# Kernel tuning notes

Hardware: AMD Instinct MI355X
Metric: run time of the kernel (lower is better)

## Reference

```python
import jax, jax.numpy as jnp
from jax import lax
import numpy as np

BN_EPS = 1e-3  # ultralytics BatchNorm2d default eps

def setup_inputs() -> dict:
    key = jax.random.key(0)
    ks = jax.random.split(key, 6)
    B, C, H, W = 16, 64, 160, 160
    E, R = 4, 16  # experts, reduced router dim = C // reduction
    return {
        "x": jax.random.normal(ks[0], (B, C, H, W), jnp.float32),
        "fc1_w": jax.random.normal(ks[1], (R, C), jnp.float32) * 0.1,
        "fc2_w": jax.random.normal(ks[2], (E, R), jnp.float32) * 0.1,
        "fc2_b": jax.random.normal(ks[3], (E,), jnp.float32) * 0.1,
        "conv_w": jax.random.normal(ks[4], (E, C, C, 3, 3), jnp.float32) * 0.05,
        "bn_gamma": jnp.ones((E, C), jnp.float32),
        "bn_beta": jnp.zeros((E, C), jnp.float32),
        "bn_mean": jax.random.normal(ks[5], (E, C), jnp.float32) * 0.1,
        "bn_var": jnp.ones((E, C), jnp.float32),
    }

def reference(x, fc1_w, fc2_w, fc2_b, conv_w, bn_gamma, bn_beta, bn_mean, bn_var):
    # Router: global avg pool -> fc1 -> relu -> fc2 -> softmax over experts
    g = jnp.mean(x, axis=(2, 3))                       # [B, C]
    h = jax.nn.relu(g @ fc1_w.T)                       # [B, R]
    w = jax.nn.softmax(h @ fc2_w.T + fc2_b, axis=1)    # [B, E]

    def expert(kernel, gamma, beta, mean, var):
        # Conv2d(bias=False, pad=k//2) + BatchNorm2d (eval) + SiLU
        y = lax.conv_general_dilated(
            x, kernel, window_strides=(1, 1), padding="SAME",
            dimension_numbers=("NCHW", "OIHW", "NCHW"))
        scale = (gamma * lax.rsqrt(var + BN_EPS))[None, :, None, None]
        shift = (beta - mean * gamma * lax.rsqrt(var + BN_EPS))[None, :, None, None]
        return jax.nn.silu(y * scale + shift)          # [B, Co, H, W]

    outs = jax.vmap(expert)(conv_w, bn_gamma, bn_beta, bn_mean, bn_var)  # [E, B, Co, H, W]
    return jnp.einsum("ebchw,be->bchw", outs, w)
```

## Files before the change

### kernel.cpp

```cpp
#include <hip/hip_runtime.h>
#include <hip/hip_bf16.h>

typedef unsigned short u16;
typedef unsigned int   u32;
typedef __attribute__((ext_vector_type(8))) short s16x8;
typedef __attribute__((ext_vector_type(16))) float f32x16;

#define BN_EPS 1e-3f
#define NB 16
#define NC 64
#define NH 160
#define NW 160
#define HP 162
#define WPD 162

#define OFF_XT 0UL
#define SZ_XT  (16UL*162*162*64*2)
#define OFF_WT (OFF_XT + SZ_XT)
#define SZ_WT  (4UL*64*9*64*2)
#define OFF_SC (OFF_WT + SZ_WT)
#define OFF_SH (OFF_SC + 1024UL)
#define OFF_WE (OFF_SH + 1024UL)
#define OFF_GP (OFF_WE + 256UL)

#define XSTRIDE 342
#define XLS_BYTES (8 * XSTRIDE * 16)
#define WLS_BYTES (2304 * 16)
#define SMEM_TOTAL (XLS_BYTES + WLS_BYTES)

__device__ __forceinline__ u16 f2bf(float f) {
    u32 u = __builtin_bit_cast(u32, f);
    u += 0x7fffu + ((u >> 16) & 1u);
    return (u16)(u >> 16);
}

__global__ void prep_all(const float* __restrict__ x, u16* __restrict__ xt,
                         float* __restrict__ gpart,
                         const float* __restrict__ cw, u16* __restrict__ wt,
                         const float* __restrict__ gamma, const float* __restrict__ beta,
                         const float* __restrict__ mean, const float* __restrict__ var,
                         float* __restrict__ scale, float* __restrict__ shift) {
    __shared__ float tile[64][33];
    int blk = blockIdx.x;
    int t = threadIdx.x;
    if (blk >= 15392) {
        int idx = (blk - 15392) * 256 + t;
        {
            int cin = idx & 7;
            int r = idx >> 3;
            int co = r & 63; r >>= 6;
            int cio = r & 3; r >>= 2;
            int tap = r % 9; r /= 9;
            int ch = r & 1;
            int e = r >> 1;
            int ci = ch * 32 + cio * 8 + cin;
            wt[idx] = f2bf(cw[(((long)(e * 64 + co)) * 64 + ci) * 9 + tap]);
        }
        if (idx < 256) {
            float sc = gamma[idx] * rsqrtf(var[idx] + BN_EPS);
            scale[idx] = sc;
            shift[idx] = beta[idx] - mean[idx] * sc;
        }
        return;
    }
    if (blk >= 12800) {
        int bb = blk - 12800;
        int hp = bb % 162, b = bb / 162;
        u32* row = (u32*)xt + (((long)b * 162 + hp) * 162) * 32;
        if (hp == 0 || hp == 161) {
            for (int i = t; i < 162 * 32; i += 256) row[i] = 0u;
        } else if (t < 64) {
            int p = (t >> 5) ? 161 : 0;
            row[p * 32 + (t & 31)] = 0u;
        }
        return;
    }
    int wt5 = blk % 5;
    int tmp = blk / 5;
    int h = tmp % 160, b = tmp / 160;
    int w0 = wt5 * 32;
    int w = t & 31, c0 = t >> 5;
#pragma unroll
    for (int i = 0; i < 8; ++i) {
        int c = c0 + 8 * i;
        tile[c][w] = x[(((long)b * 64 + c) * 160 + h) * 160 + w0 + w];
    }
    __syncthreads();
    if (t < 64) {
        float s = 0.f;
#pragma unroll
        for (int wi = 0; wi < 32; ++wi) s += tile[t][wi];
        gpart[((long)(b * 64 + t)) * 800 + h * 5 + wt5] = s;
    }
    u32* xt32 = (u32*)xt;
    long base = ((((long)b * 162 + h + 1) * 162) + (w0 + 1)) * 32;
#pragma unroll
    for (int j = 0; j < 4; ++j) {
        int idx = t + 256 * j;
        int p = idx >> 5, cp = idx & 31;
        float v0 = tile[2 * cp][p], v1 = tile[2 * cp + 1][p];
        xt32[base + p * 32 + cp] = (u32)f2bf(v0) | ((u32)f2bf(v1) << 16);
    }
}

__global__ void router16(const float* __restrict__ gpart,
                         const float* __restrict__ fc1w, const float* __restrict__ fc2w,
                         const float* __restrict__ fc2b, float* __restrict__ wexp) {
    __shared__ float part[256];
    __shared__ float gl[64];
    __shared__ float h1[16];
    int b = blockIdx.x, t = threadIdx.x;
    int c = t >> 2, q = t & 3;
    const float* gp = gpart + ((long)(b * 64 + c)) * 800;
    float s = 0.f;
    for (int i = q; i < 800; i += 4) s += gp[i];
    part[t] = s;
    __syncthreads();
    if (t < 64)
        gl[t] = (part[4 * t] + part[4 * t + 1] + part[4 * t + 2] + part[4 * t + 3])
                * (1.f / 25600.f);
    __syncthreads();
    if (t < 16) {
        float v = 0.f;
#pragma unroll
        for (int c2 = 0; c2 < 64; ++c2) v += gl[c2] * fc1w[t * 64 + c2];
        h1[t] = fmaxf(v, 0.f);
    }
    __syncthreads();
    if (t == 0) {
        float z[4];
#pragma unroll
        for (int e = 0; e < 4; ++e) {
            float v = fc2b[e];
#pragma unroll
            for (int r = 0; r < 16; ++r) v += h1[r] * fc2w[e * 16 + r];
            z[e] = v;
        }
        float m = fmaxf(fmaxf(z[0], z[1]), fmaxf(z[2], z[3]));
        float e0 = __expf(z[0] - m), e1 = __expf(z[1] - m);
        float e2 = __expf(z[2] - m), e3 = __expf(z[3] - m);
        float inv = 1.f / (e0 + e1 + e2 + e3);
        wexp[b * 4 + 0] = e0 * inv; wexp[b * 4 + 1] = e1 * inv;
        wexp[b * 4 + 2] = e2 * inv; wexp[b * 4 + 3] = e3 * inv;
    }
}

__global__ __launch_bounds__(256, 2) void conv_main(
    const u16* __restrict__ xt, const u16* __restrict__ wt,
    const float* __restrict__ scale, const float* __restrict__ shift,
    const float* __restrict__ wexp, float* __restrict__ out) {
    extern __shared__ char smem[];
    u16* xls = (u16*)smem;
    u16* wls = (u16*)(smem + XLS_BYTES);

    const int o = blockIdx.x;
    const int blk = (o & 7) * 200 + (o >> 3);
    const int wt5 = blk % 5;
    const int tmp = blk / 5;
    const int ht = tmp % 20;
    const int b = tmp / 20;
    const int h0 = ht * 8, w0 = wt5 * 32;
    const int tid = threadIdx.x;
    const int lane = tid & 63;
    const int wv = tid >> 6;
    const int l31 = lane & 31, kh = lane >> 5;
    const int r0 = 2 * wv;

    {
#pragma unroll
        for (int r = 0; r < 9; ++r) {
            int oo = r * 256 + tid;
            __builtin_amdgcn_global_load_lds(
                (const __attribute__((address_space(1))) void*)(wt + oo * 8),
                (__attribute__((address_space(3))) void*)(wls + oo * 8),
                16, 0, 0);
        }
    }
    {
        const u16* xb = xt + (long)b * HP * WPD * 64;
        for (int c = tid; c < 2720; c += 256) {
            int P = c >> 3, cg = c & 7;
            int y = P / 34, px = P - y * 34;
            const u16* src = xb + (((long)(h0 + y) * WPD) + (w0 + px)) * 64 + cg * 8;
            s16x8 v = *(const s16x8*)src;
            *(s16x8*)(&xls[(cg * XSTRIDE + P) << 3]) = v;
        }
    }

    const int oA2 = (kh * 64 + l31) << 3;
    const int oB_0 = ((kh * XSTRIDE) + (r0 + 0) * 34 + l31) << 3;
    const int oB_1 = ((kh * XSTRIDE) + (r0 + 1) * 34 + l31) << 3;

    f32x16 acc00 = (f32x16)(0.f), acc01 = (f32x16)(0.f);
    f32x16 acc10 = (f32x16)(0.f), acc11 = (f32x16)(0.f);
    f32x16 oac00 = (f32x16)(0.f), oac01 = (f32x16)(0.f);
    f32x16 oac10 = (f32x16)(0.f), oac11 = (f32x16)(0.f);

    auto epi = [&](int E) {
        const float we = wexp[(b << 2) + E];
        const float* scE = scale + (E << 6);
        const float* shE = shift + (E << 6);
#pragma unroll
        for (int j = 0; j < 16; ++j) {
            const int cob = (j & 3) + 8 * (j >> 2) + 4 * kh;
            {
                float sc = scE[cob], sh = shE[cob];
                float y0 = acc00[j] * sc + sh;
                float y1 = acc01[j] * sc + sh;
                oac00[j] += we * (y0 * __builtin_amdgcn_rcpf(1.f + __expf(-y0)));
                oac01[j] += we * (y1 * __builtin_amdgcn_rcpf(1.f + __expf(-y1)));
            }
            {
                float sc = scE[cob + 32], sh = shE[cob + 32];
                float y0 = acc10[j] * sc + sh;
                float y1 = acc11[j] * sc + sh;
                oac10[j] += we * (y0 * __builtin_amdgcn_rcpf(1.f + __expf(-y0)));
                oac11[j] += we * (y1 * __builtin_amdgcn_rcpf(1.f + __expf(-y1)));
            }
        }
        acc00 = (f32x16)(0.f); acc01 = (f32x16)(0.f);
        acc10 = (f32x16)(0.f); acc11 = (f32x16)(0.f);
    };

#pragma unroll 1
    for (int s = 0; s < 8; ++s) {
        const int ch = s & 1;
        if (s > 0) {
            __syncthreads();
            const u16* wsrc = wt + ((long)s) * 2304 * 8;
#pragma unroll
            for (int r = 0; r < 9; ++r) {
                int oo = r * 256 + tid;
                __builtin_amdgcn_global_load_lds(
                    (const __attribute__((address_space(1))) void*)(wsrc + oo * 8),
                    (__attribute__((address_space(3))) void*)(wls + oo * 8),
                    16, 0, 0);
            }
        }
        const int oBc0 = oB_0 + ((ch * 4 * XSTRIDE) << 3);
        const int oBc1 = oB_1 + ((ch * 4 * XSTRIDE) << 3);

        auto tap_body = [&](int tap) {
            const int dy = tap / 3, dx = tap - 3 * dy;
            const int pofU = (dy * 34 + dx) << 3;
            const int atU = oA2 + tap * 2048;
            s16x8 a00 = *(const s16x8*)(&wls[atU]);
            s16x8 a10 = *(const s16x8*)(&wls[atU + 256]);
            s16x8 a01 = *(const s16x8*)(&wls[atU + 1024]);
            s16x8 a11 = *(const s16x8*)(&wls[atU + 1280]);
            s16x8 b00 = *(const s16x8*)(&xls[oBc0 + pofU]);
            s16x8 b10 = *(const s16x8*)(&xls[oBc1 + pofU]);
            s16x8 b01 = *(const s16x8*)(&xls[oBc0 + pofU + 2 * XSTRIDE * 8]);
            s16x8 b11 = *(const s16x8*)(&xls[oBc1 + pofU + 2 * XSTRIDE * 8]);
            acc00 = __builtin_amdgcn_mfma_f32_32x32x16_bf16(a00, b00, acc00, 0, 0, 0);
            acc10 = __builtin_amdgcn_mfma_f32_32x32x16_bf16(a10, b00, acc10, 0, 0, 0);
            acc01 = __builtin_amdgcn_mfma_f32_32x32x16_bf16(a00, b10, acc01, 0, 0, 0);
            acc11 = __builtin_amdgcn_mfma_f32_32x32x16_bf16(a10, b10, acc11, 0, 0, 0);
            acc00 = __builtin_amdgcn_mfma_f32_32x32x16_bf16(a01, b01, acc00, 0, 0, 0);
            acc10 = __builtin_amdgcn_mfma_f32_32x32x16_bf16(a11, b01, acc10, 0, 0, 0);
            acc01 = __builtin_amdgcn_mfma_f32_32x32x16_bf16(a01, b11, acc01, 0, 0, 0);
            acc11 = __builtin_amdgcn_mfma_f32_32x32x16_bf16(a11, b11, acc11, 0, 0, 0);
        };

        if (s == 0) __builtin_amdgcn_s_waitcnt(0x070);
        else        __builtin_amdgcn_s_waitcnt(0x074);
        __builtin_amdgcn_s_barrier();
        __builtin_amdgcn_sched_barrier(0);
        if (ch == 0 && s > 0) epi((s >> 1) - 1);
#pragma unroll
        for (int tap = 0; tap < 5; ++tap) tap_body(tap);

        __builtin_amdgcn_s_waitcnt(0xF70);
        __builtin_amdgcn_s_barrier();
        __builtin_amdgcn_sched_barrier(0);
#pragma unroll
        for (int tap = 5; tap < 9; ++tap) tap_body(tap);
    }
    epi(3);

    const int yy = h0 + r0;
#pragma unroll
    for (int j = 0; j < 16; ++j) {
        const int cob = (j & 3) + 8 * (j >> 2) + 4 * kh;
        out[(((long)(b * 64 + cob)) * 160 + yy) * 160 + w0 + l31] = oac00[j];
        out[(((long)(b * 64 + cob)) * 160 + yy + 1) * 160 + w0 + l31] = oac01[j];
        out[(((long)(b * 64 + cob + 32)) * 160 + yy) * 160 + w0 + l31] = oac10[j];
        out[(((long)(b * 64 + cob + 32)) * 160 + yy + 1) * 160 + w0 + l31] = oac11[j];
    }
}

extern "C" void kernel_launch(void* const* d_in, const int* in_sizes, int n_in,
                              void* d_out, int out_size, void* d_ws, size_t ws_size,
                              hipStream_t stream) {
    const float* x = (const float*)d_in[0];
    const float* fc1w = (const float*)d_in[1];
    const float* fc2w = (const float*)d_in[2];
    const float* fc2b = (const float*)d_in[3];
    const float* convw = (const float*)d_in[4];
    const float* gamma = (const float*)d_in[5];
    const float* beta = (const float*)d_in[6];
    const float* mean = (const float*)d_in[7];
    const float* var = (const float*)d_in[8];
    float* out = (float*)d_out;
    char* ws = (char*)d_ws;
    u16* xt = (u16*)(ws + OFF_XT);
    u16* wtb = (u16*)(ws + OFF_WT);
    float* scale = (float*)(ws + OFF_SC);
    float* shift = (float*)(ws + OFF_SH);
    float* wexp = (float*)(ws + OFF_WE);
    float* gpart = (float*)(ws + OFF_GP);

    hipFuncSetAttribute((const void*)conv_main,
                        hipFuncAttributeMaxDynamicSharedMemorySize, SMEM_TOTAL);

    prep_all<<<15968, 256, 0, stream>>>(x, xt, gpart, convw, wtb,
                                        gamma, beta, mean, var, scale, shift);
    router16<<<16, 256, 0, stream>>>(gpart, fc1w, fc2w, fc2b, wexp);
    conv_main<<<1600, 256, SMEM_TOTAL, stream>>>(xt, wtb, scale, shift, wexp, out);
}
```

Before: 194.1 us.

## Reorder conv taps by dx to reuse LDS B-fragments and split router reduction

```diff
diff --git a/kernel.cpp b/kernel.cpp
--- a/kernel.cpp
+++ b/kernel.cpp
@@ -20,7 +20,8 @@
 #define SZ_WT  (4UL*64*9*64*2)
 #define OFF_SC (OFF_WT + SZ_WT)
 #define OFF_SH (OFF_SC + 1024UL)
-#define OFF_WE (OFF_SH + 1024UL)
+#define OFF_G  (OFF_SH + 1024UL)
+#define OFF_WE (OFF_G + 4096UL)
 #define OFF_GP (OFF_WE + 256UL)
 
 #define XSTRIDE 342
@@ -34,35 +35,35 @@
     return (u16)(u >> 16);
 }
 
-__global__ void prep_all(const float* __restrict__ x, u16* __restrict__ xt,
-                         float* __restrict__ gpart,
-                         const float* __restrict__ cw, u16* __restrict__ wt,
-                         const float* __restrict__ gamma, const float* __restrict__ beta,
-                         const float* __restrict__ mean, const float* __restrict__ var,
-                         float* __restrict__ scale, float* __restrict__ shift) {
+__global__ void prep_w(const float* __restrict__ cw, u16* __restrict__ wt,
+                       const float* __restrict__ gamma, const float* __restrict__ beta,
+                       const float* __restrict__ mean, const float* __restrict__ var,
+                       float* __restrict__ scale, float* __restrict__ shift) {
+    int idx = blockIdx.x * 256 + threadIdx.x;
+    if (idx < 4 * 2 * 9 * 4 * 64 * 8) {
+        int cin = idx & 7;
+        int t = idx >> 3;
+        int co = t & 63; t >>= 6;
+        int cio = t & 3; t >>= 2;
+        int pos = t % 9; t /= 9;
+        int ch = t & 1;
+        int e = t >> 1;
+        int tsp = (pos % 3) * 3 + (pos / 3);
+        int ci = ch * 32 + cio * 8 + cin;
+        wt[idx] = f2bf(cw[(((long)(e * 64 + co)) * 64 + ci) * 9 + tsp]);
+    }
+    if (idx < 256) {
+        float sc = gamma[idx] * rsqrtf(var[idx] + BN_EPS);
+        scale[idx] = sc;
+        shift[idx] = beta[idx] - mean[idx] * sc;
+    }
+}
+
+__global__ void prep_x(const float* __restrict__ x, u16* __restrict__ xt,
+                       float* __restrict__ gpart) {
     __shared__ float tile[64][33];
     int blk = blockIdx.x;
     int t = threadIdx.x;
-    if (blk >= 15392) {
-        int idx = (blk - 15392) * 256 + t;
-        {
-            int cin = idx & 7;
-            int r = idx >> 3;
-            int co = r & 63; r >>= 6;
-            int cio = r & 3; r >>= 2;
-            int tap = r % 9; r /= 9;
-            int ch = r & 1;
-            int e = r >> 1;
-            int ci = ch * 32 + cio * 8 + cin;
-            wt[idx] = f2bf(cw[(((long)(e * 64 + co)) * 64 + ci) * 9 + tap]);
-        }
-        if (idx < 256) {
-            float sc = gamma[idx] * rsqrtf(var[idx] + BN_EPS);
-            scale[idx] = sc;
-            shift[idx] = beta[idx] - mean[idx] * sc;
-        }
-        return;
-    }
     if (blk >= 12800) {
         int bb = blk - 12800;
         int hp = bb % 162, b = bb / 162;
@@ -103,42 +104,49 @@
     }
 }
 
-__global__ void router16(const float* __restrict__ gpart,
-                         const float* __restrict__ fc1w, const float* __restrict__ fc2w,
-                         const float* __restrict__ fc2b, float* __restrict__ wexp) {
-    __shared__ float part[256];
-    __shared__ float gl[64];
-    __shared__ float h1[16];
-    int b = blockIdx.x, t = threadIdx.x;
-    int c = t >> 2, q = t & 3;
-    const float* gp = gpart + ((long)(b * 64 + c)) * 800;
+__global__ void g_reduce(const float* __restrict__ gpart, float* __restrict__ g) {
+    int id = blockIdx.x;
+    int t = threadIdx.x;
     float s = 0.f;
-    for (int i = q; i < 800; i += 4) s += gp[i];
-    part[t] = s;
-    __syncthreads();
-    if (t < 64)
-        gl[t] = (part[4 * t] + part[4 * t + 1] + part[4 * t + 2] + part[4 * t + 3])
-                * (1.f / 25600.f);
+    for (int i = t; i < 800; i += 256) s += gpart[(long)id * 800 + i];
+#pragma unroll
+    for (int off = 32; off > 0; off >>= 1) s += __shfl_down(s, off, 64);
+    __shared__ float red[4];
+    if ((t & 63) == 0) red[t >> 6] = s;
+    __syncthreads();
+    if (t == 0) g[id] = (red[0] + red[1] + red[2] + red[3]) * (1.f / 25600.f);
+}
+
+__global__ void router(const float* __restrict__ g, const float* __restrict__ fc1w,
+                       const float* __restrict__ fc2w, const float* __restrict__ fc2b,
+                       float* __restrict__ wexp) {
+    __shared__ float gL[16][64];
+    __shared__ float h1[16][16];
+    __shared__ float z[16][4];
+    int t = threadIdx.x;
+    for (int i = t; i < 1024; i += 256) gL[i >> 6][i & 63] = g[i];
+    __syncthreads();
+    {
+        int b = t >> 4, r = t & 15;
+        float s = 0.f;
+#pragma unroll
+        for (int c = 0; c < 64; ++c) s += gL[b][c] * fc1w[r * 64 + c];
+        h1[b][r] = fmaxf(s, 0.f);
+    }
+    __syncthreads();
+    if (t < 64) {
+        int b = t >> 2, e = t & 3;
+        float s = fc2b[e];
+#pragma unroll
+        for (int r = 0; r < 16; ++r) s += h1[b][r] * fc2w[e * 16 + r];
+        z[b][e] = s;
+    }
     __syncthreads();
     if (t < 16) {
-        float v = 0.f;
-#pragma unroll
-        for (int c2 = 0; c2 < 64; ++c2) v += gl[c2] * fc1w[t * 64 + c2];
-        h1[t] = fmaxf(v, 0.f);
-    }
-    __syncthreads();
-    if (t == 0) {
-        float z[4];
-#pragma unroll
-        for (int e = 0; e < 4; ++e) {
-            float v = fc2b[e];
-#pragma unroll
-            for (int r = 0; r < 16; ++r) v += h1[r] * fc2w[e * 16 + r];
-            z[e] = v;
-        }
-        float m = fmaxf(fmaxf(z[0], z[1]), fmaxf(z[2], z[3]));
-        float e0 = __expf(z[0] - m), e1 = __expf(z[1] - m);
-        float e2 = __expf(z[2] - m), e3 = __expf(z[3] - m);
+        int b = t;
+        float m = fmaxf(fmaxf(z[b][0], z[b][1]), fmaxf(z[b][2], z[b][3]));
+        float e0 = __expf(z[b][0] - m), e1 = __expf(z[b][1] - m);
+        float e2 = __expf(z[b][2] - m), e3 = __expf(z[b][3] - m);
         float inv = 1.f / (e0 + e1 + e2 + e3);
         wexp[b * 4 + 0] = e0 * inv; wexp[b * 4 + 1] = e1 * inv;
         wexp[b * 4 + 2] = e2 * inv; wexp[b * 4 + 3] = e3 * inv;
@@ -188,8 +196,8 @@
     }
 
     const int oA2 = (kh * 64 + l31) << 3;
-    const int oB_0 = ((kh * XSTRIDE) + (r0 + 0) * 34 + l31) << 3;
-    const int oB_1 = ((kh * XSTRIDE) + (r0 + 1) * 34 + l31) << 3;
+    const int oBk0 = ((kh * XSTRIDE) + r0 * 34 + l31) << 3;
+    const int oBk1 = oBk0 + ((2 * XSTRIDE) << 3);
 
     f32x16 acc00 = (f32x16)(0.f), acc01 = (f32x16)(0.f);
     f32x16 acc10 = (f32x16)(0.f), acc11 = (f32x16)(0.f);
@@ -237,46 +245,56 @@
                     16, 0, 0);
             }
         }
-        const int oBc0 = oB_0 + ((ch * 4 * XSTRIDE) << 3);
-        const int oBc1 = oB_1 + ((ch * 4 * XSTRIDE) << 3);
-
-        auto tap_body = [&](int tap) {
-            const int dy = tap / 3, dx = tap - 3 * dy;
-            const int pofU = (dy * 34 + dx) << 3;
-            const int atU = oA2 + tap * 2048;
-            s16x8 a00 = *(const s16x8*)(&wls[atU]);
-            s16x8 a10 = *(const s16x8*)(&wls[atU + 256]);
-            s16x8 a01 = *(const s16x8*)(&wls[atU + 1024]);
-            s16x8 a11 = *(const s16x8*)(&wls[atU + 1280]);
-            s16x8 b00 = *(const s16x8*)(&xls[oBc0 + pofU]);
-            s16x8 b10 = *(const s16x8*)(&xls[oBc1 + pofU]);
-            s16x8 b01 = *(const s16x8*)(&xls[oBc0 + pofU + 2 * XSTRIDE * 8]);
-            s16x8 b11 = *(const s16x8*)(&xls[oBc1 + pofU + 2 * XSTRIDE * 8]);
-            acc00 = __builtin_amdgcn_mfma_f32_32x32x16_bf16(a00, b00, acc00, 0, 0, 0);
-            acc10 = __builtin_amdgcn_mfma_f32_32x32x16_bf16(a10, b00, acc10, 0, 0, 0);
-            acc01 = __builtin_amdgcn_mfma_f32_32x32x16_bf16(a00, b10, acc01, 0, 0, 0);
-            acc11 = __builtin_amdgcn_mfma_f32_32x32x16_bf16(a10, b10, acc11, 0, 0, 0);
-            acc00 = __builtin_amdgcn_mfma_f32_32x32x16_bf16(a01, b01, acc00, 0, 0, 0);
-            acc10 = __builtin_amdgcn_mfma_f32_32x32x16_bf16(a11, b01, acc10, 0, 0, 0);
-            acc01 = __builtin_amdgcn_mfma_f32_32x32x16_bf16(a01, b11, acc01, 0, 0, 0);
-            acc11 = __builtin_amdgcn_mfma_f32_32x32x16_bf16(a11, b11, acc11, 0, 0, 0);
+        const int chU = (ch * 4 * XSTRIDE) << 3;
+        const int b0U = oBk0 + chU;
+        const int b1U = oBk1 + chU;
+
+        auto dx_group = [&](int g, int pos0) {
+            const int gU = g << 3;
+            s16x8 B00 = *(const s16x8*)(&xls[b0U + gU]);
+            s16x8 B01 = *(const s16x8*)(&xls[b1U + gU]);
+            s16x8 B10 = *(const s16x8*)(&xls[b0U + gU + (34 << 3)]);
+            s16x8 B11 = *(const s16x8*)(&xls[b1U + gU + (34 << 3)]);
+            s16x8 B20 = *(const s16x8*)(&xls[b0U + gU + (68 << 3)]);
+            s16x8 B21 = *(const s16x8*)(&xls[b1U + gU + (68 << 3)]);
+            s16x8 B30 = *(const s16x8*)(&xls[b0U + gU + (102 << 3)]);
+            s16x8 B31 = *(const s16x8*)(&xls[b1U + gU + (102 << 3)]);
+#pragma unroll
+            for (int dy = 0; dy < 3; ++dy) {
+                const int atU = oA2 + (pos0 + dy) * 2048;
+                s16x8 a00 = *(const s16x8*)(&wls[atU]);
+                s16x8 a10 = *(const s16x8*)(&wls[atU + 256]);
+                s16x8 a01 = *(const s16x8*)(&wls[atU + 1024]);
+                s16x8 a11 = *(const s16x8*)(&wls[atU + 1280]);
+                s16x8 bn00 = (dy == 0) ? B00 : (dy == 1) ? B10 : B20;
+                s16x8 bn01 = (dy == 0) ? B01 : (dy == 1) ? B11 : B21;
+                s16x8 bn10 = (dy == 0) ? B10 : (dy == 1) ? B20 : B30;
+                s16x8 bn11 = (dy == 0) ? B11 : (dy == 1) ? B21 : B31;
+                acc00 = __builtin_amdgcn_mfma_f32_32x32x16_bf16(a00, bn00, acc00, 0, 0, 0);
+                acc10 = __builtin_amdgcn_mfma_f32_32x32x16_bf16(a10, bn00, acc10, 0, 0, 0);
+                acc01 = __builtin_amdgcn_mfma_f32_32x32x16_bf16(a00, bn10, acc01, 0, 0, 0);
+                acc11 = __builtin_amdgcn_mfma_f32_32x32x16_bf16(a10, bn10, acc11, 0, 0, 0);
+                acc00 = __builtin_amdgcn_mfma_f32_32x32x16_bf16(a01, bn01, acc00, 0, 0, 0);
+                acc10 = __builtin_amdgcn_mfma_f32_32x32x16_bf16(a11, bn01, acc10, 0, 0, 0);
+                acc01 = __builtin_amdgcn_mfma_f32_32x32x16_bf16(a01, bn11, acc01, 0, 0, 0);
+                acc11 = __builtin_amdgcn_mfma_f32_32x32x16_bf16(a11, bn11, acc11, 0, 0, 0);
+            }
         };
 
         if (s == 0) __builtin_amdgcn_s_waitcnt(0x070);
-        else        __builtin_amdgcn_s_waitcnt(0x074);
+        else        __builtin_amdgcn_s_waitcnt(0xF73);
         __builtin_amdgcn_s_barrier();
         __builtin_amdgcn_sched_barrier(0);
-        if (ch == 0 && s > 0) epi((s >> 1) - 1);
-#pragma unroll
-        for (int tap = 0; tap < 5; ++tap) tap_body(tap);
+        dx_group(0, 0);
+        dx_group(1, 3);
 
         __builtin_amdgcn_s_waitcnt(0xF70);
         __builtin_amdgcn_s_barrier();
         __builtin_amdgcn_sched_barrier(0);
-#pragma unroll
-        for (int tap = 5; tap < 9; ++tap) tap_body(tap);
-    }
-    epi(3);
+        dx_group(2, 6);
+
+        if (ch == 1) epi(s >> 1);
+    }
 
     const int yy = h0 + r0;
 #pragma unroll
@@ -307,14 +325,16 @@
     u16* wtb = (u16*)(ws + OFF_WT);
     float* scale = (float*)(ws + OFF_SC);
     float* shift = (float*)(ws + OFF_SH);
+    float* g = (float*)(ws + OFF_G);
     float* wexp = (float*)(ws + OFF_WE);
     float* gpart = (float*)(ws + OFF_GP);
 
     hipFuncSetAttribute((const void*)conv_main,
                         hipFuncAttributeMaxDynamicSharedMemorySize, SMEM_TOTAL);
 
-    prep_all<<<15968, 256, 0, stream>>>(x, xt, gpart, convw, wtb,
-                                        gamma, beta, mean, var, scale, shift);
-    router16<<<16, 256, 0, stream>>>(gpart, fc1w, fc2w, fc2b, wexp);
+    prep_w<<<576, 256, 0, stream>>>(convw, wtb, gamma, beta, mean, var, scale, shift);
+    prep_x<<<15392, 256, 0, stream>>>(x, xt, gpart);
+    g_reduce<<<1024, 256, 0, stream>>>(gpart, g);
+    router<<<1, 256, 0, stream>>>(g, fc1w, fc2w, fc2b, wexp);
     conv_main<<<1600, 256, SMEM_TOTAL, stream>>>(xt, wtb, scale, shift, wexp, out);
 }
```

Result: faster. 182.4 us (-6.0%).

## Fold BN scale into weights, reorder taps by column for B-fragment reuse

Applied to the files above, without the earlier changes.

```diff
diff --git a/kernel.cpp b/kernel.cpp
--- a/kernel.cpp
+++ b/kernel.cpp
@@ -18,8 +18,7 @@
 #define SZ_XT  (16UL*162*162*64*2)
 #define OFF_WT (OFF_XT + SZ_XT)
 #define SZ_WT  (4UL*64*9*64*2)
-#define OFF_SC (OFF_WT + SZ_WT)
-#define OFF_SH (OFF_SC + 1024UL)
+#define OFF_SH (OFF_WT + SZ_WT)
 #define OFF_WE (OFF_SH + 1024UL)
 #define OFF_GP (OFF_WE + 256UL)
 
@@ -39,7 +38,7 @@
                          const float* __restrict__ cw, u16* __restrict__ wt,
                          const float* __restrict__ gamma, const float* __restrict__ beta,
                          const float* __restrict__ mean, const float* __restrict__ var,
-                         float* __restrict__ scale, float* __restrict__ shift) {
+                         float* __restrict__ shift) {
     __shared__ float tile[64][33];
     int blk = blockIdx.x;
     int t = threadIdx.x;
@@ -50,15 +49,17 @@
             int r = idx >> 3;
             int co = r & 63; r >>= 6;
             int cio = r & 3; r >>= 2;
-            int tap = r % 9; r /= 9;
+            int pos = r % 9; r /= 9;
             int ch = r & 1;
             int e = r >> 1;
+            int tsp = (pos % 3) * 3 + (pos / 3);
             int ci = ch * 32 + cio * 8 + cin;
-            wt[idx] = f2bf(cw[(((long)(e * 64 + co)) * 64 + ci) * 9 + tap]);
+            int ec = e * 64 + co;
+            float sc = gamma[ec] * rsqrtf(var[ec] + BN_EPS);
+            wt[idx] = f2bf(cw[(((long)ec) * 64 + ci) * 9 + tsp] * sc);
         }
         if (idx < 256) {
             float sc = gamma[idx] * rsqrtf(var[idx] + BN_EPS);
-            scale[idx] = sc;
             shift[idx] = beta[idx] - mean[idx] * sc;
         }
         return;
@@ -90,7 +91,7 @@
         float s = 0.f;
 #pragma unroll
         for (int wi = 0; wi < 32; ++wi) s += tile[t][wi];
-        gpart[((long)(b * 64 + t)) * 800 + h * 5 + wt5] = s;
+        gpart[(((long)b * 800) + h * 5 + wt5) * 64 + t] = s;
     }
     u32* xt32 = (u32*)xt;
     long base = ((((long)b * 162 + h + 1) * 162) + (w0 + 1)) * 32;
@@ -103,21 +104,21 @@
     }
 }
 
-__global__ void router16(const float* __restrict__ gpart,
+__global__ void finish16(const float* __restrict__ gpart,
                          const float* __restrict__ fc1w, const float* __restrict__ fc2w,
                          const float* __restrict__ fc2b, float* __restrict__ wexp) {
     __shared__ float part[256];
     __shared__ float gl[64];
     __shared__ float h1[16];
     int b = blockIdx.x, t = threadIdx.x;
-    int c = t >> 2, q = t & 3;
-    const float* gp = gpart + ((long)(b * 64 + c)) * 800;
+    int c = t & 63, q = t >> 6;
+    const float* gp = gpart + (long)b * 800 * 64;
     float s = 0.f;
-    for (int i = q; i < 800; i += 4) s += gp[i];
+    for (int i = q; i < 800; i += 4) s += gp[i * 64 + c];
     part[t] = s;
     __syncthreads();
     if (t < 64)
-        gl[t] = (part[4 * t] + part[4 * t + 1] + part[4 * t + 2] + part[4 * t + 3])
+        gl[t] = (part[t] + part[t + 64] + part[t + 128] + part[t + 192])
                 * (1.f / 25600.f);
     __syncthreads();
     if (t < 16) {
@@ -147,7 +148,7 @@
 
 __global__ __launch_bounds__(256, 2) void conv_main(
     const u16* __restrict__ xt, const u16* __restrict__ wt,
-    const float* __restrict__ scale, const float* __restrict__ shift,
+    const float* __restrict__ shift,
     const float* __restrict__ wexp, float* __restrict__ out) {
     extern __shared__ char smem[];
     u16* xls = (u16*)smem;
@@ -188,8 +189,8 @@
     }
 
     const int oA2 = (kh * 64 + l31) << 3;
-    const int oB_0 = ((kh * XSTRIDE) + (r0 + 0) * 34 + l31) << 3;
-    const int oB_1 = ((kh * XSTRIDE) + (r0 + 1) * 34 + l31) << 3;
+    const int oBk0 = ((kh * XSTRIDE) + r0 * 34 + l31) << 3;
+    const int oBk1 = oBk0 + ((2 * XSTRIDE) << 3);
 
     f32x16 acc00 = (f32x16)(0.f), acc01 = (f32x16)(0.f);
     f32x16 acc10 = (f32x16)(0.f), acc11 = (f32x16)(0.f);
@@ -198,22 +199,21 @@
 
     auto epi = [&](int E) {
         const float we = wexp[(b << 2) + E];
-        const float* scE = scale + (E << 6);
         const float* shE = shift + (E << 6);
 #pragma unroll
         for (int j = 0; j < 16; ++j) {
             const int cob = (j & 3) + 8 * (j >> 2) + 4 * kh;
             {
-                float sc = scE[cob], sh = shE[cob];
-                float y0 = acc00[j] * sc + sh;
-                float y1 = acc01[j] * sc + sh;
+                float sh = shE[cob];
+                float y0 = acc00[j] + sh;
+                float y1 = acc01[j] + sh;
                 oac00[j] += we * (y0 * __builtin_amdgcn_rcpf(1.f + __expf(-y0)));
                 oac01[j] += we * (y1 * __builtin_amdgcn_rcpf(1.f + __expf(-y1)));
             }
             {
-                float sc = scE[cob + 32], sh = shE[cob + 32];
-                float y0 = acc10[j] * sc + sh;
-                float y1 = acc11[j] * sc + sh;
+                float sh = shE[cob + 32];
+                float y0 = acc10[j] + sh;
+                float y1 = acc11[j] + sh;
                 oac10[j] += we * (y0 * __builtin_amdgcn_rcpf(1.f + __expf(-y0)));
                 oac11[j] += we * (y1 * __builtin_amdgcn_rcpf(1.f + __expf(-y1)));
             }
@@ -237,46 +237,60 @@
                     16, 0, 0);
             }
         }
-        const int oBc0 = oB_0 + ((ch * 4 * XSTRIDE) << 3);
-        const int oBc1 = oB_1 + ((ch * 4 * XSTRIDE) << 3);
-
-        auto tap_body = [&](int tap) {
-            const int dy = tap / 3, dx = tap - 3 * dy;
-            const int pofU = (dy * 34 + dx) << 3;
-            const int atU = oA2 + tap * 2048;
-            s16x8 a00 = *(const s16x8*)(&wls[atU]);
-            s16x8 a10 = *(const s16x8*)(&wls[atU + 256]);
-            s16x8 a01 = *(const s16x8*)(&wls[atU + 1024]);
-            s16x8 a11 = *(const s16x8*)(&wls[atU + 1280]);
-            s16x8 b00 = *(const s16x8*)(&xls[oBc0 + pofU]);
-            s16x8 b10 = *(const s16x8*)(&xls[oBc1 + pofU]);
-            s16x8 b01 = *(const s16x8*)(&xls[oBc0 + pofU + 2 * XSTRIDE * 8]);
-            s16x8 b11 = *(const s16x8*)(&xls[oBc1 + pofU + 2 * XSTRIDE * 8]);
-            acc00 = __builtin_amdgcn_mfma_f32_32x32x16_bf16(a00, b00, acc00, 0, 0, 0);
-            acc10 = __builtin_amdgcn_mfma_f32_32x32x16_bf16(a10, b00, acc10, 0, 0, 0);
-            acc01 = __builtin_amdgcn_mfma_f32_32x32x16_bf16(a00, b10, acc01, 0, 0, 0);
-            acc11 = __builtin_amdgcn_mfma_f32_32x32x16_bf16(a10, b10, acc11, 0, 0, 0);
-            acc00 = __builtin_amdgcn_mfma_f32_32x32x16_bf16(a01, b01, acc00, 0, 0, 0);
-            acc10 = __builtin_amdgcn_mfma_f32_32x32x16_bf16(a11, b01, acc10, 0, 0, 0);
-            acc01 = __builtin_amdgcn_mfma_f32_32x32x16_bf16(a01, b11, acc01, 0, 0, 0);
-            acc11 = __builtin_amdgcn_mfma_f32_32x32x16_bf16(a11, b11, acc11, 0, 0, 0);
+        const int chU = (ch * 4 * XSTRIDE) << 3;
+        const int b0U = oBk0 + chU;
+        const int b1U = oBk1 + chU;
+
+        auto dx_group = [&](int g, int pos0) {
+            const int gU = g << 3;
+            s16x8 B00 = *(const s16x8*)(&xls[b0U + gU]);
+            s16x8 B01 = *(const s16x8*)(&xls[b1U + gU]);
+            s16x8 B10 = *(const s16x8*)(&xls[b0U + gU + (34 << 3)]);
+            s16x8 B11 = *(const s16x8*)(&xls[b1U + gU + (34 << 3)]);
+            s16x8 B20 = *(const s16x8*)(&xls[b0U + gU + (68 << 3)]);
+            s16x8 B21 = *(const s16x8*)(&xls[b1U + gU + (68 << 3)]);
+            s16x8 B30 = *(const s16x8*)(&xls[b0U + gU + (102 << 3)]);
+            s16x8 B31 = *(const s16x8*)(&xls[b1U + gU + (102 << 3)]);
+#pragma unroll
+            for (int dy = 0; dy < 3; ++dy) {
+                const int atU = oA2 + (pos0 + dy) * 2048;
+                s16x8 a00 = *(const s16x8*)(&wls[atU]);
+                s16x8 a10 = *(const s16x8*)(&wls[atU + 256]);
+                s16x8 a01 = *(const s16x8*)(&wls[atU + 1024]);
+                s16x8 a11 = *(const s16x8*)(&wls[atU + 1280]);
+                s16x8 bn00 = (dy == 0) ? B00 : (dy == 1) ? B10 : B20;
+                s16x8 bn01 = (dy == 0) ? B01 : (dy == 1) ? B11 : B21;
+                s16x8 bn10 = (dy == 0) ? B10 : (dy == 1) ? B20 : B30;
+                s16x8 bn11 = (dy == 0) ? B11 : (dy == 1) ? B21 : B31;
+                acc00 = __builtin_amdgcn_mfma_f32_32x32x16_bf16(a00, bn00, acc00, 0, 0, 0);
+                acc10 = __builtin_amdgcn_mfma_f32_32x32x16_bf16(a10, bn00, acc10, 0, 0, 0);
+                acc01 = __builtin_amdgcn_mfma_f32_32x32x16_bf16(a00, bn10, acc01, 0, 0, 0);
+                acc11 = __builtin_amdgcn_mfma_f32_32x32x16_bf16(a10, bn10, acc11, 0, 0, 0);
+                acc00 = __builtin_amdgcn_mfma_f32_32x32x16_bf16(a01, bn01, acc00, 0, 0, 0);
+                acc10 = __builtin_amdgcn_mfma_f32_32x32x16_bf16(a11, bn01, acc10, 0, 0, 0);
+                acc01 = __builtin_amdgcn_mfma_f32_32x32x16_bf16(a01, bn11, acc01, 0, 0, 0);
+                acc11 = __builtin_amdgcn_mfma_f32_32x32x16_bf16(a11, bn11, acc11, 0, 0, 0);
+            }
         };
 
         if (s == 0) __builtin_amdgcn_s_waitcnt(0x070);
-        else        __builtin_amdgcn_s_waitcnt(0x074);
+        else        __builtin_amdgcn_s_waitcnt(0xF76);
         __builtin_amdgcn_s_barrier();
         __builtin_amdgcn_sched_barrier(0);
-        if (ch == 0 && s > 0) epi((s >> 1) - 1);
-#pragma unroll
-        for (int tap = 0; tap < 5; ++tap) tap_body(tap);
+        dx_group(0, 0);
+
+        __builtin_amdgcn_s_waitcnt(0xF73);
+        __builtin_amdgcn_s_barrier();
+        __builtin_amdgcn_sched_barrier(0);
+        dx_group(1, 3);
 
         __builtin_amdgcn_s_waitcnt(0xF70);
         __builtin_amdgcn_s_barrier();
         __builtin_amdgcn_sched_barrier(0);
-#pragma unroll
-        for (int tap = 5; tap < 9; ++tap) tap_body(tap);
-    }
-    epi(3);
+        dx_group(2, 6);
+
+        if (ch == 1) epi(s >> 1);
+    }
 
     const int yy = h0 + r0;
 #pragma unroll
@@ -305,7 +319,6 @@
     char* ws = (char*)d_ws;
     u16* xt = (u16*)(ws + OFF_XT);
     u16* wtb = (u16*)(ws + OFF_WT);
-    float* scale = (float*)(ws + OFF_SC);
     float* shift = (float*)(ws + OFF_SH);
     float* wexp = (float*)(ws + OFF_WE);
     float* gpart = (float*)(ws + OFF_GP);
@@ -314,7 +327,7 @@
                         hipFuncAttributeMaxDynamicSharedMemorySize, SMEM_TOTAL);
 
     prep_all<<<15968, 256, 0, stream>>>(x, xt, gpart, convw, wtb,
-                                        gamma, beta, mean, var, scale, shift);
-    router16<<<16, 256, 0, stream>>>(gpart, fc1w, fc2w, fc2b, wexp);
-    conv_main<<<1600, 256, SMEM_TOTAL, stream>>>(xt, wtb, scale, shift, wexp, out);
-}
+                                        gamma, beta, mean, var, shift);
+    finish16<<<16, 256, 0, stream>>>(gpart, fc1w, fc2w, fc2b, wexp);
+    conv_main<<<1600, 256, SMEM_TOTAL, stream>>>(xt, wtb, shift, wexp, out);
+}
```

After: 209.8 us. 1.08x slower.
